# Kernel tuning notes

Measured on AMD Instinct MI355X. Metric: run time of the kernel, lower is better.

## Reference

```python
import jax, jax.numpy as jnp
import numpy as np

B, S, H, D, HID = 1024, 64, 32, 32, 1024
COMP = 256          # smolgen compress_size
TOK = 32            # smolgen token_compress out dim
LN_EPS = 1e-5


def _xavier(key, shape):
    fan_in, fan_out = shape[0], shape[-1]
    std = np.sqrt(2.0 / (fan_in + fan_out))
    return jax.random.normal(key, shape, dtype=jnp.float32) * std


def setup_inputs() -> dict:
    key = jax.random.key(0)
    ks = jax.random.split(key, 12)
    x = jax.random.normal(ks[0], (B, S, HID), dtype=jnp.float32)
    # attention projections (stored [in, out], no bias on qkv)
    Wq = _xavier(ks[1], (HID, H * D))
    Wk = _xavier(ks[2], (HID, H * D))
    Wv = _xavier(ks[3], (HID, H * D))
    Wo = _xavier(ks[4], (H * D, HID))
    bo = jnp.zeros((HID,), dtype=jnp.float32)
    pos_bias = jnp.zeros((H, S, S), dtype=jnp.float32)
    # smolgen params
    tc_W = _xavier(ks[5], (HID, TOK))                  # token_compress, no bias
    pc_W = _xavier(ks[6], (S * TOK, COMP))             # position_compress linear
    pc_b = jnp.zeros((COMP,), dtype=jnp.float32)
    ln_g = jnp.ones((COMP,), dtype=jnp.float32)        # LayerNorm gamma
    ln_b = jnp.zeros((COMP,), dtype=jnp.float32)       # LayerNorm beta
    hp_W = jax.vmap(lambda k: _xavier(k, (COMP, COMP)))(jax.random.split(ks[7], H))  # [H,COMP,COMP]
    hp_b = jnp.zeros((H, COMP), dtype=jnp.float32)
    alp_W = _xavier(ks[8], (COMP, S * S))              # attention_logits_proj
    alp_b = jnp.zeros((S * S,), dtype=jnp.float32)
    return dict(x=x, Wq=Wq, Wk=Wk, Wv=Wv, Wo=Wo, bo=bo, pos_bias=pos_bias,
                tc_W=tc_W, pc_W=pc_W, pc_b=pc_b, ln_g=ln_g, ln_b=ln_b,
                hp_W=hp_W, hp_b=hp_b, alp_W=alp_W, alp_b=alp_b)


def _smolgen(x, tc_W, pc_W, pc_b, ln_g, ln_b, hp_W, hp_b, alp_W, alp_b):
    b = x.shape[0]
    flat = (x @ tc_W).reshape(b, S * TOK)              # [B, 64*32]
    pv = jax.nn.relu(flat @ pc_W + pc_b)               # [B, COMP]
    mu = jnp.mean(pv, axis=-1, keepdims=True)
    var = jnp.mean(jnp.square(pv - mu), axis=-1, keepdims=True)
    pv = (pv - mu) * jax.lax.rsqrt(var + LN_EPS) * ln_g + ln_b
    # per-head projections, vectorized over heads
    hv = jnp.einsum('bc,hcd->bhd', pv, hp_W) + hp_b    # [B, H, COMP]
    logits = jnp.einsum('bhd,de->bhe', hv, alp_W) + alp_b
    return logits.reshape(b, H, S, S)


def reference(x, Wq, Wk, Wv, Wo, bo, pos_bias, tc_W, pc_W, pc_b, ln_g, ln_b,
              hp_W, hp_b, alp_W, alp_b):
    b = x.shape[0]
    scale = 1.0 / np.sqrt(D)
    q = (x @ Wq).reshape(b, S, H, D).transpose(0, 2, 1, 3)  # [B,H,S,D]
    k = (x @ Wk).reshape(b, S, H, D).transpose(0, 2, 1, 3)
    v = (x @ Wv).reshape(b, S, H, D).transpose(0, 2, 1, 3)
    scores = jnp.einsum('bhqd,bhkd->bhqk', q, k) * scale
    scores = scores + pos_bias[None]
    scores = scores + _smolgen(x, tc_W, pc_W, pc_b, ln_g, ln_b, hp_W, hp_b, alp_W, alp_b)
    attn = jax.nn.softmax(scores, axis=-1)
    out = jnp.einsum('bhqk,bhkd->bhqd', attn, v)             # [B,H,S,D]
    out = out.transpose(0, 2, 1, 3).reshape(b, S, H * D)
    return out @ Wo + bo
```

## Files before the change

kernel.cpp:

```cpp
#include <hip/hip_runtime.h>
#include <hip/hip_bf16.h>
#include <cstdint>
#include <cstddef>

typedef __attribute__((ext_vector_type(4))) float f32x4;
typedef __attribute__((ext_vector_type(8))) short short8;
typedef unsigned short u16;
typedef __attribute__((ext_vector_type(8))) unsigned short u16x8;
typedef __attribute__((ext_vector_type(4))) unsigned short u16x4;

__device__ __forceinline__ u16 f2bf(float f) {
  union { float f; unsigned u; } v; v.f = f;
  unsigned r = v.u + 0x7FFFu + ((v.u >> 16) & 1u);
  return (u16)(r >> 16);
}
__device__ __forceinline__ float bf2f(u16 h) {
  union { unsigned u; float f; } v; v.u = ((unsigned)h) << 16;
  return v.f;
}
__device__ __forceinline__ void gload16(const u16* g, const u16* l) {
  __builtin_amdgcn_global_load_lds((const __attribute__((address_space(1))) void*)g,
                                   (__attribute__((address_space(3))) void*)l, 16, 0, 0);
}
__device__ __forceinline__ void fenced_barrier() {
  __builtin_amdgcn_sched_barrier(0);
  __builtin_amdgcn_s_barrier();
  __builtin_amdgcn_sched_barrier(0);
}

__global__ __launch_bounds__(256) void prep_w2t(
    const float* __restrict__ Wq, const float* __restrict__ Wk, const float* __restrict__ Wv,
    const float* __restrict__ tc, u16* __restrict__ W2t)
{
  __shared__ float t[32][33];
  const int tx = threadIdx.x, ty = threadIdx.y;
  const int k0 = blockIdx.x * 32, n0 = blockIdx.y * 32;
  const float* src = nullptr; int col = 0, sw = 0;
  if      (n0 < 1024) { src = Wq; col = n0;        sw = 1024; }
  else if (n0 < 2048) { src = Wk; col = n0 - 1024; sw = 1024; }
  else if (n0 < 3072) { src = Wv; col = n0 - 2048; sw = 1024; }
  else if (n0 < 3104) { src = tc; col = n0 - 3072; sw = 32;   }
  if (src) {
    #pragma unroll
    for (int r = 0; r < 4; r++) {
      int k = k0 + ty + r * 8;
      t[ty + r * 8][tx] = src[(size_t)k * sw + col + tx];
    }
  }
  __syncthreads();
  #pragma unroll
  for (int r = 0; r < 4; r++) {
    int n = n0 + ty + r * 8, k = k0 + tx;
    u16 v = src ? f2bf(t[tx][ty + r * 8]) : (u16)0;
    W2t[(size_t)n * 1024 + k] = v;
  }
}

__global__ __launch_bounds__(256) void transpose_bf(
    const float* __restrict__ src, u16* __restrict__ dst, int R, int C)
{
  __shared__ float t[32][33];
  const int tx = threadIdx.x, ty = threadIdx.y;
  const size_t zoff = (size_t)blockIdx.z * R * C;
  src += zoff; dst += zoff;
  const int c0 = blockIdx.x * 32, r0 = blockIdx.y * 32;
  #pragma unroll
  for (int r = 0; r < 4; r++)
    t[ty + r * 8][tx] = src[(size_t)(r0 + ty + r * 8) * C + c0 + tx];
  __syncthreads();
  #pragma unroll
  for (int r = 0; r < 4; r++)
    dst[(size_t)(c0 + ty + r * 8) * R + r0 + tx] = f2bf(t[tx][ty + r * 8]);
}

__global__ __launch_bounds__(256) void cvt_x(const float* __restrict__ x, u16* __restrict__ A2)
{
  size_t i = (size_t)blockIdx.x * 256 + threadIdx.x;
  f32x4 v = ((const f32x4*)x)[i];
  u16x4 o;
  #pragma unroll
  for (int j = 0; j < 4; j++) o[j] = f2bf(v[j]);
  ((u16x4*)A2)[i] = o;
}

template<int MODE>
__global__ __launch_bounds__(512, 2) void gemm_p(
    const u16* __restrict__ A, const u16* __restrict__ Bt, int K,
    void* __restrict__ o0, void* __restrict__ o1, void* __restrict__ o2, void* __restrict__ o3,
    const float* __restrict__ bias0, const float* __restrict__ bias1)
{
  __shared__ __align__(16) u16 lds[4][16384];
  const int tid = threadIdx.x;
  const int wid = tid >> 6, lane = tid & 63;
  const int wm = wid >> 2, wn = wid & 3;
  const int g = lane >> 4, l15 = lane & 15;

  const int GX = gridDim.x;
  const int nwg = GX * (int)gridDim.y;
  const int lin = (int)blockIdx.y * GX + (int)blockIdx.x;
  const int swz = (lin & 7) * (nwg >> 3) + (lin >> 3);
  const int bn = swz % GX, bm = swz / GX;

  const int lR = lane >> 3;
  const int logi = (lane & 7) ^ lR;
  const int shb = logi >> 2;
  const int sg = logi & 3;

  const u16* pA0 = A + (size_t)(bm * 256 + shb * 128 + (wid * 2 + 0) * 8 + lR) * K + sg * 8;
  const u16* pA1 = A + (size_t)(bm * 256 + shb * 128 + (wid * 2 + 1) * 8 + lR) * K + sg * 8;
  const u16* pB0 = Bt + (size_t)(bn * 256 + shb * 128 + (wid * 2 + 0) * 8 + lR) * K + sg * 8;
  const u16* pB1 = Bt + (size_t)(bn * 256 + shb * 128 + (wid * 2 + 1) * 8 + lR) * K + sg * 8;

  const int aRd = l15 * 64 + ((((wm << 2) | g) ^ (l15 & 7)) << 3);
  const int bRd = 8192 + ((wn & 1) * 64 + l15) * 64 + (((((wn >> 1) << 2) | g) ^ (l15 & 7)) << 3);

  f32x4 acc[8][4];
  #pragma unroll
  for (int i = 0; i < 8; i++)
    #pragma unroll
    for (int j = 0; j < 4; j++)
      #pragma unroll
      for (int r = 0; r < 4; r++) acc[i][j][r] = 0.f;

  const int NT = K >> 5;

#define STG_A(buf, kt) do { \
    gload16(pA0 + (size_t)(kt) * 32, &lds[buf][(wid * 2 + 0) * 512]); \
    gload16(pA1 + (size_t)(kt) * 32, &lds[buf][(wid * 2 + 1) * 512]); } while (0)
#define STG_B(buf, kt) do { \
    gload16(pB0 + (size_t)(kt) * 32, &lds[buf][8192 + (wid * 2 + 0) * 512]); \
    gload16(pB1 + (size_t)(kt) * 32, &lds[buf][8192 + (wid * 2 + 1) * 512]); } while (0)

  STG_A(0, 0); STG_B(0, 0);
  STG_A(1, 1); STG_B(1, 1);

  for (int t = 0; t < NT; t++) {
    const int rb = t & 3;
    const int wb = (t + 2) & 3;
    const bool more = (t + 2) < NT;

    if (t + 1 < NT) asm volatile("s_waitcnt vmcnt(4)" ::: "memory");
    else            asm volatile("s_waitcnt vmcnt(0)" ::: "memory");
    fenced_barrier();

    short8 af[8], bfr[4];
    #pragma unroll
    for (int f = 0; f < 4; f++) af[f] = *(const short8*)&lds[rb][aRd + f * 1024];
    #pragma unroll
    for (int n = 0; n < 4; n++) bfr[n] = *(const short8*)&lds[rb][bRd + n * 1024];
    if (more) STG_A(wb, t + 2);
    asm volatile("s_waitcnt lgkmcnt(0)" ::: "memory");
    __builtin_amdgcn_sched_barrier(0);
    __builtin_amdgcn_s_setprio(1);
    #pragma unroll
    for (int f = 0; f < 4; f++)
      #pragma unroll
      for (int n = 0; n < 4; n++)
        acc[f][n] = __builtin_amdgcn_mfma_f32_16x16x32_bf16(af[f], bfr[n], acc[f][n], 0, 0, 0);
    __builtin_amdgcn_s_setprio(0);

    #pragma unroll
    for (int f = 4; f < 8; f++) af[f] = *(const short8*)&lds[rb][aRd + f * 1024];
    if (more) STG_B(wb, t + 2);
    asm volatile("s_waitcnt lgkmcnt(0)" ::: "memory");
    __builtin_amdgcn_sched_barrier(0);
    __builtin_amdgcn_s_setprio(1);
    #pragma unroll
    for (int f = 4; f < 8; f++)
      #pragma unroll
      for (int n = 0; n < 4; n++)
        acc[f][n] = __builtin_amdgcn_mfma_f32_16x16x32_bf16(af[f], bfr[n], acc[f][n], 0, 0, 0);
    __builtin_amdgcn_s_setprio(0);
  }
#undef STG_A
#undef STG_B

  const int lr = lane >> 4, lc = lane & 15;
  #pragma unroll
  for (int fm = 0; fm < 8; fm++) {
    #pragma unroll
    for (int fn = 0; fn < 4; fn++) {
      #pragma unroll
      for (int r = 0; r < 4; r++) {
        int gm = bm * 256 + wm * 128 + fm * 16 + lr * 4 + r;
        int gn = bn * 256 + wn * 64 + fn * 16 + lc;
        float val = acc[fm][fn][r];
        if (MODE == 0) {
          int b = gm >> 6, s = gm & 63;
          if (gn < 3072) {
            int which = gn >> 10, hh = (gn >> 5) & 31, d = gn & 31;
            u16* dst = (which == 0) ? (u16*)o0 : (which == 1) ? (u16*)o1 : (u16*)o2;
            dst[(((size_t)b * 32 + hh) * 64 + s) * 32 + d] = f2bf(val);
          } else if (gn < 3104) {
            ((u16*)o3)[(size_t)b * 2048 + s * 32 + (gn - 3072)] = f2bf(val);
          }
        } else if (MODE == 3) {
          ((u16*)o0)[(size_t)gm * 4096 + gn] = f2bf(val + bias0[gn] + bias1[(gm & 31) * 4096 + gn]);
        } else {
          ((float*)o0)[(size_t)gm * 1024 + gn] = val + bias0[gn];
        }
      }
    }
  }
}

template<int MODE>
__global__ __launch_bounds__(256) void gemm_bt(
    const u16* __restrict__ A, const u16* __restrict__ Bt, int K,
    void* __restrict__ o0, const float* __restrict__ bias0)
{
  __shared__ __align__(16) u16 lA[128 * 32];
  __shared__ __align__(16) u16 lB[128 * 32];
  const int tid = threadIdx.x;
  const int wid = tid >> 6, lane = tid & 63;
  const int wm = wid >> 1, wn = wid & 1;
  const int bn = blockIdx.x, bm = blockIdx.y;
  if (MODE == 2) Bt += (size_t)blockIdx.z * 256 * 256;

  f32x4 acc[4][4];
  #pragma unroll
  for (int i = 0; i < 4; i++)
    #pragma unroll
    for (int j = 0; j < 4; j++)
      #pragma unroll
      for (int r = 0; r < 4; r++) acc[i][j][r] = 0.f;

  const u16* Arow = A + (size_t)(bm * 128) * K;
  const u16* Brow = Bt + (size_t)(bn * 128) * K;

  for (int k0 = 0; k0 < K; k0 += 32) {
    #pragma unroll
    for (int i = 0; i < 2; i++) {
      int c = wid * 128 + i * 64 + lane;
      int row = c >> 2, col = (c & 3) * 8;
      gload16(Arow + (size_t)row * K + k0 + col, &lA[(wid * 128 + i * 64) * 8]);
      gload16(Brow + (size_t)row * K + k0 + col, &lB[(wid * 128 + i * 64) * 8]);
    }
    __syncthreads();
    short8 af[4], bfr[4];
    #pragma unroll
    for (int f = 0; f < 4; f++) {
      af[f]  = *(const short8*)&lA[(wm * 64 + f * 16 + (lane & 15)) * 32 + (lane >> 4) * 8];
      bfr[f] = *(const short8*)&lB[(wn * 64 + f * 16 + (lane & 15)) * 32 + (lane >> 4) * 8];
    }
    #pragma unroll
    for (int fm = 0; fm < 4; fm++)
      #pragma unroll
      for (int fn = 0; fn < 4; fn++)
        acc[fm][fn] = __builtin_amdgcn_mfma_f32_16x16x32_bf16(af[fm], bfr[fn], acc[fm][fn], 0, 0, 0);
    __syncthreads();
  }

  const int lr = lane >> 4, lc = lane & 15;
  #pragma unroll
  for (int fm = 0; fm < 4; fm++) {
    #pragma unroll
    for (int fn = 0; fn < 4; fn++) {
      #pragma unroll
      for (int r = 0; r < 4; r++) {
        int gm = bm * 128 + wm * 64 + fm * 16 + lr * 4 + r;
        int gn = bn * 128 + wn * 64 + fn * 16 + lc;
        float val = acc[fm][fn][r];
        if (MODE == 1) {
          float v = val + bias0[gn];
          ((float*)o0)[(size_t)gm * 256 + gn] = v > 0.f ? v : 0.f;
        } else if (MODE == 2) {
          int h = blockIdx.z;
          ((u16*)o0)[((size_t)gm * 32 + h) * 256 + gn] = f2bf(val + bias0[h * 256 + gn]);
        }
      }
    }
  }
}

__global__ __launch_bounds__(256) void ln_kernel(
    const float* __restrict__ pv, const float* __restrict__ g, const float* __restrict__ b2,
    u16* __restrict__ out)
{
  __shared__ float red[256];
  const int bi = blockIdx.x, t = threadIdx.x;
  float v = pv[(size_t)bi * 256 + t];
  red[t] = v; __syncthreads();
  #pragma unroll
  for (int o = 128; o > 0; o >>= 1) { if (t < o) red[t] += red[t + o]; __syncthreads(); }
  float mu = red[0] * (1.f / 256.f);
  __syncthreads();
  float dv = v - mu;
  red[t] = dv * dv; __syncthreads();
  #pragma unroll
  for (int o = 128; o > 0; o >>= 1) { if (t < o) red[t] += red[t + o]; __syncthreads(); }
  float var = red[0] * (1.f / 256.f);
  float rs = rsqrtf(var + 1e-5f);
  out[(size_t)bi * 256 + t] = f2bf(dv * rs * g[t] + b2[t]);
}

__global__ __launch_bounds__(64) void attn_mfma(
    const u16* __restrict__ qb, const u16* __restrict__ kb, const u16* __restrict__ vb,
    const u16* __restrict__ lg, u16* __restrict__ aout)
{
  __shared__ __align__(16) u16 vT[32 * 64];
  __shared__ __align__(16) u16 Pl[64 * 64];
  const int bid = blockIdx.x;
  const int lane = threadIdx.x;
  const int g = lane >> 4, l15 = lane & 15;
  const size_t base = (size_t)bid * 2048;

  {
    const u16* vrow = vb + base + lane * 32;
    u16x8 vv[4];
    #pragma unroll
    for (int c = 0; c < 4; c++) vv[c] = *(const u16x8*)(vrow + c * 8);
    #pragma unroll
    for (int d = 0; d < 32; d++)
      vT[d * 64 + (lane ^ ((d & 7) << 3))] = vv[d >> 3][d & 7];
  }

  short8 qf[4], kf[4];
  #pragma unroll
  for (int t = 0; t < 4; t++) {
    qf[t] = *(const short8*)(qb + base + (size_t)(t * 16 + l15) * 32 + g * 8);
    kf[t] = *(const short8*)(kb + base + (size_t)(t * 16 + l15) * 32 + g * 8);
  }

  f32x4 s[4][4];
  #pragma unroll
  for (int tm = 0; tm < 4; tm++)
    #pragma unroll
    for (int tn = 0; tn < 4; tn++)
      #pragma unroll
      for (int r = 0; r < 4; r++) s[tm][tn][r] = 0.f;
  #pragma unroll
  for (int tm = 0; tm < 4; tm++)
    #pragma unroll
    for (int tn = 0; tn < 4; tn++)
      s[tm][tn] = __builtin_amdgcn_mfma_f32_16x16x32_bf16(kf[tm], qf[tn], s[tm][tn], 0, 0, 0);

  const float scale = 0.17677669529663687f;
  float inv4[4];
  const u16* lbase = lg + (size_t)bid * 4096;
  #pragma unroll
  for (int tn = 0; tn < 4; tn++) {
    const int q = tn * 16 + l15;
    float mx = -1e30f;
    #pragma unroll
    for (int tm = 0; tm < 4; tm++) {
      u16x4 u = *(const u16x4*)(lbase + (size_t)q * 64 + tm * 16 + g * 4);
      #pragma unroll
      for (int r = 0; r < 4; r++) {
        s[tm][tn][r] = s[tm][tn][r] * scale + bf2f(u[r]);
        mx = fmaxf(mx, s[tm][tn][r]);
      }
    }
    mx = fmaxf(mx, __shfl_xor(mx, 16));
    mx = fmaxf(mx, __shfl_xor(mx, 32));
    float sm = 0.f;
    #pragma unroll
    for (int tm = 0; tm < 4; tm++)
      #pragma unroll
      for (int r = 0; r < 4; r++) {
        float e = __expf(s[tm][tn][r] - mx);
        s[tm][tn][r] = e;
        sm += e;
      }
    sm += __shfl_xor(sm, 16);
    sm += __shfl_xor(sm, 32);
    inv4[tn] = 1.f / sm;
    #pragma unroll
    for (int tm = 0; tm < 4; tm++) {
      u16x4 p;
      #pragma unroll
      for (int r = 0; r < 4; r++) p[r] = f2bf(s[tm][tn][r]);
      *(u16x4*)&Pl[q * 64 + ((tm * 16 + g * 4) ^ ((q & 7) << 3))] = p;
    }
  }
  __syncthreads();

  f32x4 o[2][4];
  #pragma unroll
  for (int md = 0; md < 2; md++)
    #pragma unroll
    for (int tn = 0; tn < 4; tn++)
      #pragma unroll
      for (int r = 0; r < 4; r++) o[md][tn][r] = 0.f;
  #pragma unroll
  for (int ks = 0; ks < 2; ks++) {
    short8 vf2[2], pf[4];
    #pragma unroll
    for (int md = 0; md < 2; md++)
      vf2[md] = *(const short8*)&vT[(md * 16 + l15) * 64 + ((ks * 32 + g * 8) ^ ((l15 & 7) << 3))];
    #pragma unroll
    for (int tn = 0; tn < 4; tn++)
      pf[tn] = *(const short8*)&Pl[(tn * 16 + l15) * 64 + ((ks * 32 + g * 8) ^ ((l15 & 7) << 3))];
    #pragma unroll
    for (int md = 0; md < 2; md++)
      #pragma unroll
      for (int tn = 0; tn < 4; tn++)
        o[md][tn] = __builtin_amdgcn_mfma_f32_16x16x32_bf16(vf2[md], pf[tn], o[md][tn], 0, 0, 0);
  }

  const int b = bid >> 5, h = bid & 31;
  #pragma unroll
  for (int md = 0; md < 2; md++) {
    #pragma unroll
    for (int tn = 0; tn < 4; tn++) {
      const int q = tn * 16 + l15, d0 = md * 16 + g * 4;
      u16x4 u;
      #pragma unroll
      for (int r = 0; r < 4; r++) u[r] = f2bf(o[md][tn][r] * inv4[tn]);
      *(u16x4*)(aout + ((size_t)(b * 64 + q)) * 1024 + h * 32 + d0) = u;
    }
  }
}

extern "C" void kernel_launch(void* const* d_in, const int* in_sizes, int n_in,
                              void* d_out, int out_size, void* d_ws, size_t ws_size,
                              hipStream_t stream) {
  const float* x       = (const float*)d_in[0];
  const float* Wq      = (const float*)d_in[1];
  const float* Wk      = (const float*)d_in[2];
  const float* Wv      = (const float*)d_in[3];
  const float* Wo      = (const float*)d_in[4];
  const float* bo      = (const float*)d_in[5];
  const float* pos_b   = (const float*)d_in[6];
  const float* tc_W    = (const float*)d_in[7];
  const float* pc_W    = (const float*)d_in[8];
  const float* pc_b    = (const float*)d_in[9];
  const float* ln_g    = (const float*)d_in[10];
  const float* ln_b    = (const float*)d_in[11];
  const float* hp_W    = (const float*)d_in[12];
  const float* hp_b    = (const float*)d_in[13];
  const float* alp_W   = (const float*)d_in[14];
  const float* alp_b   = (const float*)d_in[15];
  float* out = (float*)d_out;

  char* w = (char*)d_ws;
  u16* A2     = (u16*)w;
  u16* logits = (u16*)w;              w += 268435456;
  u16* qb     = (u16*)w;              w += 134217728;
  u16* kb     = (u16*)w;              w += 134217728;
  u16* vb     = (u16*)w;              w += 134217728;
  u16* aout   = (u16*)w;              w += 134217728;
  u16* W2t    = (u16*)w;              w += (size_t)3328 * 1024 * 2;
  u16* pcWt   = (u16*)w;              w += (size_t)256 * 2048 * 2;
  u16* hpWt   = (u16*)w;              w += (size_t)32 * 256 * 256 * 2;
  u16* alpWt  = (u16*)w;              w += (size_t)4096 * 256 * 2;
  u16* WoT    = (u16*)w;              w += (size_t)1024 * 1024 * 2;
  u16* flatb  = (u16*)w;              w += (size_t)1024 * 2048 * 2;
  float* pvtmp= (float*)w;            w += (size_t)1024 * 256 * 4;
  u16* pvb    = (u16*)w;              w += (size_t)1024 * 256 * 2;
  u16* hvb    = (u16*)w;              w += (size_t)32768 * 256 * 2;

  prep_w2t    <<<dim3(32, 104),    dim3(32, 8), 0, stream>>>(Wq, Wk, Wv, tc_W, W2t);
  transpose_bf<<<dim3(8, 64, 1),   dim3(32, 8), 0, stream>>>(pc_W, pcWt, 2048, 256);
  transpose_bf<<<dim3(8, 8, 32),   dim3(32, 8), 0, stream>>>(hp_W, hpWt, 256, 256);
  transpose_bf<<<dim3(128, 8, 1),  dim3(32, 8), 0, stream>>>(alp_W, alpWt, 256, 4096);
  transpose_bf<<<dim3(32, 32, 1),  dim3(32, 8), 0, stream>>>(Wo, WoT, 1024, 1024);
  cvt_x       <<<65536, 256, 0, stream>>>(x, A2);

  gemm_p<0> <<<dim3(13, 256),    512, 0, stream>>>(A2, W2t, 1024, qb, kb, vb, flatb, nullptr, nullptr);
  gemm_bt<1><<<dim3(2, 8),       256, 0, stream>>>(flatb, pcWt, 2048, pvtmp, pc_b);
  ln_kernel <<<1024, 256, 0, stream>>>(pvtmp, ln_g, ln_b, pvb);
  gemm_bt<2><<<dim3(2, 8, 32),   256, 0, stream>>>(pvb, hpWt, 256, hvb, hp_b);
  gemm_p<3> <<<dim3(16, 128),    512, 0, stream>>>(hvb, alpWt, 256, logits, nullptr, nullptr, nullptr, alp_b, pos_b);
  attn_mfma <<<32768, 64, 0, stream>>>(qb, kb, vb, logits, aout);
  gemm_p<4> <<<dim3(4, 256),     512, 0, stream>>>(aout, WoT, 1024, out, nullptr, nullptr, nullptr, bo, nullptr);
}
```

Before: 1.086 ms.

## Restructure GEMM main loop into a 4-slot, 8-phase software pipeline

Replaces the per-k-tile double-issue loop in the bf16 MFMA GEMM with an unrolled loop over four k-tiles at a time. Each k-tile is split into two phases over 4-row fragment groups, with the A and B prefetches for tile k+3 onward spread across phases and explicit LDS slot offsets. The aim is to interleave global-to-LDS loads more finely with MFMA work and to wait on vmcnt only every two tiles. In exchange it adds a barrier around every phase and assumes K is a multiple of 128.

```diff
diff --git a/kernel.cpp b/kernel.cpp
--- a/kernel.cpp
+++ b/kernel.cpp
@@ -89,7 +89,7 @@
     void* __restrict__ o0, void* __restrict__ o1, void* __restrict__ o2, void* __restrict__ o3,
     const float* __restrict__ bias0, const float* __restrict__ bias1)
 {
-  __shared__ __align__(16) u16 lds[4][16384];
+  __shared__ __align__(16) u16 lds[65536];
   const int tid = threadIdx.x;
   const int wid = tid >> 6, lane = tid & 63;
   const int wm = wid >> 2, wn = wid & 3;
@@ -111,8 +111,16 @@
   const u16* pB0 = Bt + (size_t)(bn * 256 + shb * 128 + (wid * 2 + 0) * 8 + lR) * K + sg * 8;
   const u16* pB1 = Bt + (size_t)(bn * 256 + shb * 128 + (wid * 2 + 1) * 8 + lR) * K + sg * 8;
 
-  const int aRd = l15 * 64 + ((((wm << 2) | g) ^ (l15 & 7)) << 3);
-  const int bRd = 8192 + ((wn & 1) * 64 + l15) * 64 + (((((wn >> 1) << 2) | g) ^ (l15 & 7)) << 3);
+  const int aRd0 = l15 * 64 + ((((wm << 2) | g) ^ (l15 & 7)) << 3);
+  int bRd[4];
+  #pragma unroll
+  for (int n = 0; n < 4; n++) {
+    const int Rb = (wn & 1) * 64 + n * 16 + l15;
+    bRd[n] = Rb * 64 + (((((wn >> 1) << 2) | g) ^ (l15 & 7)) << 3);
+  }
+
+  enum { A00 = 0, A01 = 8192, A10 = 16384, A11 = 24576,
+         B00 = 32768, B01 = 40960, B10 = 49152, B11 = 57344 };
 
   f32x4 acc[8][4];
   #pragma unroll
@@ -122,56 +130,60 @@
       #pragma unroll
       for (int r = 0; r < 4; r++) acc[i][j][r] = 0.f;
 
-  const int NT = K >> 5;
-
-#define STG_A(buf, kt) do { \
-    gload16(pA0 + (size_t)(kt) * 32, &lds[buf][(wid * 2 + 0) * 512]); \
-    gload16(pA1 + (size_t)(kt) * 32, &lds[buf][(wid * 2 + 1) * 512]); } while (0)
-#define STG_B(buf, kt) do { \
-    gload16(pB0 + (size_t)(kt) * 32, &lds[buf][8192 + (wid * 2 + 0) * 512]); \
-    gload16(pB1 + (size_t)(kt) * 32, &lds[buf][8192 + (wid * 2 + 1) * 512]); } while (0)
-
-  STG_A(0, 0); STG_B(0, 0);
-  STG_A(1, 1); STG_B(1, 1);
-
-  for (int t = 0; t < NT; t++) {
-    const int rb = t & 3;
-    const int wb = (t + 2) & 3;
-    const bool more = (t + 2) < NT;
-
-    if (t + 1 < NT) asm volatile("s_waitcnt vmcnt(4)" ::: "memory");
-    else            asm volatile("s_waitcnt vmcnt(0)" ::: "memory");
-    fenced_barrier();
-
-    short8 af[8], bfr[4];
-    #pragma unroll
-    for (int f = 0; f < 4; f++) af[f] = *(const short8*)&lds[rb][aRd + f * 1024];
-    #pragma unroll
-    for (int n = 0; n < 4; n++) bfr[n] = *(const short8*)&lds[rb][bRd + n * 1024];
-    if (more) STG_A(wb, t + 2);
-    asm volatile("s_waitcnt lgkmcnt(0)" ::: "memory");
-    __builtin_amdgcn_sched_barrier(0);
-    __builtin_amdgcn_s_setprio(1);
-    #pragma unroll
-    for (int f = 0; f < 4; f++)
-      #pragma unroll
-      for (int n = 0; n < 4; n++)
-        acc[f][n] = __builtin_amdgcn_mfma_f32_16x16x32_bf16(af[f], bfr[n], acc[f][n], 0, 0, 0);
-    __builtin_amdgcn_s_setprio(0);
-
-    #pragma unroll
-    for (int f = 4; f < 8; f++) af[f] = *(const short8*)&lds[rb][aRd + f * 1024];
-    if (more) STG_B(wb, t + 2);
-    asm volatile("s_waitcnt lgkmcnt(0)" ::: "memory");
-    __builtin_amdgcn_sched_barrier(0);
-    __builtin_amdgcn_s_setprio(1);
-    #pragma unroll
-    for (int f = 4; f < 8; f++)
-      #pragma unroll
-      for (int n = 0; n < 4; n++)
-        acc[f][n] = __builtin_amdgcn_mfma_f32_16x16x32_bf16(af[f], bfr[n], acc[f][n], 0, 0, 0);
-    __builtin_amdgcn_s_setprio(0);
-  }
+  const int NT32 = K >> 5;
+  const int NI = NT32 >> 2;
+
+#define STG_A(slot, kt) { gload16(pA0 + (size_t)(kt) * 32, &lds[(slot) + (wid * 2 + 0) * 512]); \
+                          gload16(pA1 + (size_t)(kt) * 32, &lds[(slot) + (wid * 2 + 1) * 512]); }
+#define STG_B(slot, kt) { gload16(pB0 + (size_t)(kt) * 32, &lds[(slot) + (wid * 2 + 0) * 512]); \
+                          gload16(pB1 + (size_t)(kt) * 32, &lds[(slot) + (wid * 2 + 1) * 512]); }
+
+#define PHASE(ASL, BSL, FMG, LOADB, STG_STMT, WAITK) do {                        \
+    if (LOADB) {                                                                  \
+      _Pragma("unroll")                                                           \
+      for (int n_ = 0; n_ < 4; n_++)                                              \
+        bfr[n_] = *(const short8*)&lds[(BSL) + bRd[n_]];                          \
+    }                                                                             \
+    _Pragma("unroll")                                                             \
+    for (int f_ = 0; f_ < 4; f_++)                                                \
+      af[f_] = *(const short8*)&lds[(ASL) + aRd0 + ((FMG) * 4 + f_) * 1024];      \
+    STG_STMT;                                                                     \
+    if ((WAITK) == 1) asm volatile("s_waitcnt vmcnt(4)" ::: "memory");            \
+    if ((WAITK) == 2) asm volatile("s_waitcnt vmcnt(0)" ::: "memory");            \
+    fenced_barrier();                                                             \
+    asm volatile("s_waitcnt lgkmcnt(0)" ::: "memory");                            \
+    __builtin_amdgcn_sched_barrier(0);                                            \
+    __builtin_amdgcn_s_setprio(1);                                                \
+    _Pragma("unroll")                                                             \
+    for (int f_ = 0; f_ < 4; f_++)                                                \
+      _Pragma("unroll")                                                           \
+      for (int n_ = 0; n_ < 4; n_++)                                              \
+        acc[(FMG) * 4 + f_][n_] = __builtin_amdgcn_mfma_f32_16x16x32_bf16(        \
+            af[f_], bfr[n_], acc[(FMG) * 4 + f_][n_], 0, 0, 0);                   \
+    __builtin_amdgcn_s_setprio(0);                                                \
+    fenced_barrier();                                                             \
+  } while (0)
+
+  STG_A(A00, 0); STG_B(B00, 0);
+  STG_A(A01, 1); STG_B(B01, 1);
+  STG_A(A10, 2); STG_B(B10, 2);
+  asm volatile("s_waitcnt vmcnt(4)" ::: "memory");
+  fenced_barrier();
+
+  for (int i = 0; i < NI; i++) {
+    const int k4 = i * 4;
+    const bool more = (i + 1 < NI);
+    short8 af[4], bfr[4];
+    PHASE(A00, B00, 0, true,  STG_A(A11, k4 + 3),              0);
+    PHASE(A00, B00, 1, false, STG_B(B11, k4 + 3),              0);
+    PHASE(A01, B01, 0, true,  if (more) STG_A(A00, k4 + 4),    0);
+    PHASE(A01, B01, 1, false, if (more) STG_B(B00, k4 + 4),    (more ? 1 : 2));
+    PHASE(A10, B10, 0, true,  if (more) STG_A(A01, k4 + 5),    0);
+    PHASE(A10, B10, 1, false, if (more) STG_B(B01, k4 + 5),    0);
+    PHASE(A11, B11, 0, true,  if (more) STG_A(A10, k4 + 6),    0);
+    PHASE(A11, B11, 1, false, if (more) STG_B(B10, k4 + 6),    (more ? 1 : 2));
+  }
+#undef PHASE
 #undef STG_A
 #undef STG_B
 
```

After: 1.489 ms. +37.1%, slower.
